# Optimization experiments

Hardware: AMD Instinct MI355X
Metric: run time of the kernel (lower is better)

Reference implementation:

```python
import jax, jax.numpy as jnp
import numpy as np

N = 10000      # nodes
E = 320000     # edges
H = 128        # hidden_features
GF = 12        # graph-level features
L = 6          # gnn layers
EPS = 1e-5


def _glorot(key, shape):
    fan_in = shape[0]
    return (jax.random.normal(key, shape, jnp.float32) / np.sqrt(fan_in)).astype(jnp.float32)


def periodic_difference(x_i, x_j, domain):
    diff = x_i - x_j
    # (1 - 2*(x_i < x_j)) * domain  ==  +domain if x_i >= x_j else -domain
    shift = jnp.where(x_i < x_j, -domain, domain)
    diff_shifted = diff - shift
    return jnp.where(jnp.abs(diff) < jnp.abs(diff_shifted), diff, diff_shifted)


def _mlp2_relu(x, W1, b1, W2, b2):
    # Linear -> ReLU -> Linear -> ReLU
    return jax.nn.relu(jax.nn.relu(x @ W1 + b1) @ W2 + b2)


def setup_inputs() -> dict:
    key = jax.random.key(0)
    ks = jax.random.split(key, 32)
    inp = {
        "v": jax.random.normal(ks[0], (N, 6), jnp.float32),
        "pos": jax.random.uniform(ks[1], (N, 3), jnp.float32),
        "r": jax.random.uniform(ks[2], (N, 1), jnp.float32),
        "domain": jnp.ones((3,), jnp.float32),
        "t": jax.random.uniform(ks[3], (1,), jnp.float32),
        "x_global": jax.random.normal(ks[4], (4,), jnp.float32),
        "domain_next": jnp.ones((3,), jnp.float32),
        "t_next": jax.random.uniform(ks[5], (1,), jnp.float32),
        "edge_index": jax.random.randint(ks[6], (2, E), 0, N, jnp.int32),
        "batch": jnp.zeros((N,), jnp.int32),
    }
    # embedding MLP: 19 -> H -> H
    inp["emb_W1"] = _glorot(ks[7], (19, H)); inp["emb_b1"] = jnp.zeros((H,), jnp.float32)
    inp["emb_W2"] = _glorot(ks[8], (H, H)); inp["emb_b2"] = jnp.zeros((H,), jnp.float32)
    # per-layer message net: 157 -> H -> H ; update net: 268 -> H -> H
    msg_in = H + GF + 3 + 2 * (6 + 1)   # 157
    upd_in = H + H + GF                 # 268
    inp["msg_W1"] = jnp.stack([_glorot(jax.random.fold_in(ks[9], i), (msg_in, H)) for i in range(L)])
    inp["msg_b1"] = jnp.zeros((L, H), jnp.float32)
    inp["msg_W2"] = jnp.stack([_glorot(jax.random.fold_in(ks[10], i), (H, H)) for i in range(L)])
    inp["msg_b2"] = jnp.zeros((L, H), jnp.float32)
    inp["upd_W1"] = jnp.stack([_glorot(jax.random.fold_in(ks[11], i), (upd_in, H)) for i in range(L)])
    inp["upd_b1"] = jnp.zeros((L, H), jnp.float32)
    inp["upd_W2"] = jnp.stack([_glorot(jax.random.fold_in(ks[12], i), (H, H)) for i in range(L)])
    inp["upd_b2"] = jnp.zeros((L, H), jnp.float32)
    # output MLP: H -> H -> 9 ; macro MLP: H -> H -> 3
    inp["out_W1"] = _glorot(ks[13], (H, H)); inp["out_b1"] = jnp.zeros((H,), jnp.float32)
    inp["out_W2"] = _glorot(ks[14], (H, 9)); inp["out_b2"] = jnp.zeros((9,), jnp.float32)
    inp["mac_W1"] = _glorot(ks[15], (H, H)); inp["mac_b1"] = jnp.zeros((H,), jnp.float32)
    inp["mac_W2"] = _glorot(ks[16], (H, 3)); inp["mac_b2"] = jnp.zeros((3,), jnp.float32)
    return inp


def reference(v, pos, r, domain, t, x_global, domain_next, t_next, edge_index, batch,
              emb_W1, emb_b1, emb_W2, emb_b2,
              msg_W1, msg_b1, msg_W2, msg_b2,
              upd_W1, upd_b1, upd_W2, upd_b2,
              out_W1, out_b1, out_W2, out_b2,
              mac_W1, mac_b1, mac_W2, mac_b2):
    n = v.shape[0]
    gf = jnp.concatenate([domain, t, x_global, domain_next, t_next])          # [12]
    gf_n = jnp.broadcast_to(gf, (n, GF))
    node_features = jnp.concatenate([pos, v], axis=1)                         # [N, 9]

    # embedding (positions excluded)
    h = _mlp2_relu(jnp.concatenate([r, v, gf_n], axis=1), emb_W1, emb_b1, emb_W2, emb_b2)

    src, dst = edge_index[0], edge_index[1]   # j = source, i = target (PyG default)
    gf_e = jnp.broadcast_to(gf, (src.shape[0], GF))
    counts = jax.ops.segment_sum(jnp.ones(src.shape, h.dtype), dst, num_segments=N)
    inv_counts = (1.0 / jnp.maximum(counts, 1.0))[:, None]

    pos_diff = periodic_difference(pos[dst], pos[src], domain)                # [E, 3]
    v_i, v_j, r_i, r_j = v[dst], v[src], r[dst], r[src]

    for l in range(L):
        h_i, h_j = h[dst], h[src]
        msg_in = jnp.concatenate([h_i - h_j, v_i, v_j, r_i, r_j, pos_diff, gf_e], axis=1)
        m = _mlp2_relu(msg_in, msg_W1[l], msg_b1[l], msg_W2[l], msg_b2[l])    # [E, H]
        agg = jax.ops.segment_sum(m, dst, num_segments=N) * inv_counts        # scatter-mean
        upd_in = jnp.concatenate([h, agg, gf_n], axis=1)
        u = _mlp2_relu(upd_in, upd_W1[l], upd_b1[l], upd_W2[l], upd_b2[l])
        h = u + h                                                              # residual (in==out)
        # InstanceNorm over each graph (single graph here), biased variance
        mu = h.mean(axis=0, keepdims=True)
        var = h.var(axis=0, keepdims=True)
        h = (h - mu) / jnp.sqrt(var + EPS)

    prediction = jax.nn.relu(h @ out_W1 + out_b1) @ out_W2 + out_b2 + node_features
    pred_x = jnp.remainder(prediction[:, :3], domain_next)
    pred_v = prediction[:, 3:]
    h_mean = h.mean(axis=0)                                                    # global mean pool, 1 graph
    pred_macro = jax.nn.relu(h_mean @ mac_W1 + mac_b1) @ mac_W2 + mac_b2
    return pred_x, pred_v, pred_macro
```

## Files before the change

kernel.cpp:

```cpp
#include <hip/hip_runtime.h>
#include <hip/hip_bf16.h>

#define NN 10000
#define NE 320000
#define HD 128
#define NL 6
#define EPSV 1e-5f

typedef _Float16 half8  __attribute__((ext_vector_type(8)));
typedef _Float16 half4v __attribute__((ext_vector_type(4)));
typedef __fp16   pk2    __attribute__((ext_vector_type(2)));
typedef float    f32x4  __attribute__((ext_vector_type(4)));

__device__ __forceinline__ float relu_(float x){ return fmaxf(x, 0.0f); }

#define LGKM_BAR() do { asm volatile("s_waitcnt lgkmcnt(0)" ::: "memory"); __builtin_amdgcn_s_barrier(); } while(0)

__device__ __forceinline__ void stats_(const float* __restrict__ s, const float* __restrict__ q,
                                       int idx, float& m, float& rs){
  m = s[idx]*(1.0f/NN);
  float var = q[idx]*(1.0f/NN) - m*m;
  rs = rsqrtf(fmaxf(var,0.0f)+EPSV);
}

__device__ __forceinline__ void pksplit4_(const f32x4& a, uint2& hi, uint2& lo){
  pk2 ha = __builtin_amdgcn_cvt_pkrtz(a[0], a[1]);
  pk2 hb = __builtin_amdgcn_cvt_pkrtz(a[2], a[3]);
  pk2 la = __builtin_amdgcn_cvt_pkrtz(a[0]-(float)ha[0], a[1]-(float)ha[1]);
  pk2 lb = __builtin_amdgcn_cvt_pkrtz(a[2]-(float)hb[0], a[3]-(float)hb[1]);
  hi.x = __builtin_bit_cast(unsigned int, ha);
  hi.y = __builtin_bit_cast(unsigned int, hb);
  lo.x = __builtin_bit_cast(unsigned int, la);
  lo.y = __builtin_bit_cast(unsigned int, lb);
}


__global__ void k_degree(const int* __restrict__ dst, int* __restrict__ counts){
  int e = blockIdx.x*256 + threadIdx.x;
  if (e < NE) atomicAdd(&counts[dst[e]], 1);
}

__global__ void k_scan(const int* __restrict__ counts, int* __restrict__ offs, float* __restrict__ invc){
  __shared__ int lds[1024];
  __shared__ int base_s;
  int tid = threadIdx.x;
  if (tid==0) base_s = 0;
  __syncthreads();
  for (int start=0; start<NN; start+=1024){
    int i = start+tid;
    int vv = (i<NN)? counts[i] : 0;
    lds[tid]=vv; __syncthreads();
    for (int off=1; off<1024; off<<=1){
      int t = (tid>=off)? lds[tid-off] : 0;
      __syncthreads();
      lds[tid] += t;
      __syncthreads();
    }
    int incl = lds[tid];
    if (i<NN){
      offs[i] = base_s + incl - vv;
      invc[i] = 1.0f / fmaxf((float)vv, 1.0f);
    }
    __syncthreads();
    if (tid==1023) base_s += lds[1023];
    __syncthreads();
  }
  if (tid==0) offs[NN] = base_s;
}

__global__ void k_place(const int* __restrict__ src, const int* __restrict__ dst,
                        const int* __restrict__ offs, int* __restrict__ cursor, int* __restrict__ csr){
  int e = blockIdx.x*256 + threadIdx.x;
  if (e < NE){
    int d = dst[e];
    int p = atomicAdd(&cursor[d], 1);
    csr[offs[d]+p] = src[e];
  }
}


__global__ void k_biasfold(const float* __restrict__ dom, const float* __restrict__ tt,
                           const float* __restrict__ xg, const float* __restrict__ domn,
                           const float* __restrict__ tn,
                           const float* __restrict__ embW1, const float* __restrict__ embB1,
                           const float* __restrict__ msgW1, const float* __restrict__ msgB1,
                           const float* __restrict__ updW1, const float* __restrict__ updB1,
                           float* __restrict__ b1eff, float* __restrict__ s0, float* __restrict__ q0){
  float gf[12];
  gf[0]=dom[0]; gf[1]=dom[1]; gf[2]=dom[2]; gf[3]=tt[0];
  gf[4]=xg[0]; gf[5]=xg[1]; gf[6]=xg[2]; gf[7]=xg[3];
  gf[8]=domn[0]; gf[9]=domn[1]; gf[10]=domn[2]; gf[11]=tn[0];
  int b = blockIdx.x, t = threadIdx.x;
  if (b==0){
    float s = embB1[t];
    #pragma unroll
    for (int k=0;k<12;++k) s += gf[k]*embW1[(7+k)*HD + t];
    b1eff[t] = s;
  } else if (b<=6){
    int l=b-1;
    float s = msgB1[l*HD+t];
    #pragma unroll
    for (int k=0;k<12;++k) s += gf[k]*msgW1[((size_t)l*157 + 145+k)*HD + t];
    b1eff[(1+l)*HD + t] = s;
  } else if (b<=12){
    int l=b-7;
    float s = updB1[l*HD+t];
    #pragma unroll
    for (int k=0;k<12;++k) s += gf[k]*updW1[((size_t)l*268 + 256+k)*HD + t];
    b1eff[(7+l)*HD + t] = s;
  } else {
    s0[t] = 0.f;
    q0[t] = (float)NN * (1.0f - EPSV);
  }
}


__global__ __launch_bounds__(512,1) void k_embed(
    const float* __restrict__ r, const float* __restrict__ v,
    const float* __restrict__ W1, const float* __restrict__ b1e,
    const float* __restrict__ W2, const float* __restrict__ b2,
    float* __restrict__ hb){
  __shared__ alignas(16) _Float16 Ahi[16*136];
  __shared__ alignas(16) _Float16 Alo[16*136];
  int tid = threadIdx.x;
  int n0 = blockIdx.x*16;
  if (tid < 256){
    int node = tid>>4, chunk = tid&15;
    int n = n0 + node;
    int f = chunk*8;
    float in7[7];
    in7[0]=r[n];
    #pragma unroll
    for (int k=0;k<6;++k) in7[1+k]=v[n*6+k];
    half8 ah, al;
    #pragma unroll
    for (int j=0;j<8;++j){
      float z = b1e[f+j];
      #pragma unroll
      for (int k=0;k<7;++k) z += in7[k]*W1[k*HD + f+j];
      float a = fmaxf(z, 0.f);
      _Float16 h = (_Float16)a;
      ah[j] = h; al[j] = (_Float16)(a - (float)h);
    }
    *(half8*)&Ahi[node*136 + f] = ah;
    *(half8*)&Alo[node*136 + f] = al;
  }
  int wid = tid>>6, lane = tid&63, g = lane>>4, c = lane&15;
  int col = 16*wid + c;
  half8 bh[4], bl[4];
  #pragma unroll
  for (int ks=0; ks<4; ++ks){
    half8 fh, fl;
    #pragma unroll
    for (int j=0;j<8;++j){
      float w = W2[(size_t)(ks*32 + g*8 + j)*HD + col];
      _Float16 h = (_Float16)w;
      fh[j]=h; fl[j]=(_Float16)(w - (float)h);
    }
    bh[ks]=fh; bl[ks]=fl;
  }
  float b2c = b2[col];
  f32x4 zero4 = {0.f,0.f,0.f,0.f};
  __syncthreads();
  f32x4 d = zero4;
  #pragma unroll
  for (int ks=0; ks<4; ++ks){
    half8 ah = *(const half8*)&Ahi[c*136 + ks*32 + g*8];
    half8 al = *(const half8*)&Alo[c*136 + ks*32 + g*8];
    d = __builtin_amdgcn_mfma_f32_16x16x32_f16(ah, bh[ks], d, 0,0,0);
    d = __builtin_amdgcn_mfma_f32_16x16x32_f16(al, bh[ks], d, 0,0,0);
    d = __builtin_amdgcn_mfma_f32_16x16x32_f16(ah, bl[ks], d, 0,0,0);
  }
  #pragma unroll
  for (int jj=0;jj<4;++jj){
    int n = n0 + g*4 + jj;
    hb[(size_t)n*HD + col] = fmaxf(d[jj] + b2c, 0.f);
  }
}


__global__ __launch_bounds__(512,1) void k_hW(
    const float* __restrict__ hb, const float* __restrict__ Ss, const float* __restrict__ Sq,
    const float* __restrict__ v, const float* __restrict__ r,
    const float* __restrict__ W, const float* __restrict__ b1e,
    float* __restrict__ P, float* __restrict__ Q){
  __shared__ alignas(16) _Float16 Xhi[16*136];
  __shared__ alignas(16) _Float16 Xlo[16*136];
  int tid = threadIdx.x;
  int n0 = blockIdx.x*16;
  if (tid < 256){
    int node = tid>>4, chunk = tid&15;
    int n = n0 + node;
    int f = chunk*8;
    half8 xh, xl;
    #pragma unroll
    for (int j=0;j<8;++j){
      float m, rs; stats_(Ss, Sq, f+j, m, rs);
      float x = (hb[(size_t)n*HD + f+j] - m) * rs;
      _Float16 h = (_Float16)x;
      xh[j] = h; xl[j] = (_Float16)(x - (float)h);
    }
    *(half8*)&Xhi[node*136 + f] = xh;
    *(half8*)&Xlo[node*136 + f] = xl;
  }
  int wid = tid>>6, lane = tid&63, g = lane>>4, c = lane&15;
  int col = 16*wid + c;
  half8 bh[4], bl[4];
  #pragma unroll
  for (int ks=0; ks<4; ++ks){
    half8 fh, fl;
    #pragma unroll
    for (int j=0;j<8;++j){
      float w = W[(size_t)(ks*32 + g*8 + j)*HD + col];
      _Float16 h = (_Float16)w;
      fh[j]=h; fl[j]=(_Float16)(w - (float)h);
    }
    bh[ks]=fh; bl[ks]=fl;
  }
  float wvi[6], wvj[6];
  #pragma unroll
  for (int x=0;x<6;++x){
    wvi[x]=W[(size_t)(128+x)*HD+col];
    wvj[x]=W[(size_t)(134+x)*HD+col];
  }
  float wri=W[(size_t)140*HD+col], wrj=W[(size_t)141*HD+col];
  float b1c=b1e[col];
  f32x4 zero4 = {0.f,0.f,0.f,0.f};
  __syncthreads();
  f32x4 d = zero4;
  #pragma unroll
  for (int ks=0; ks<4; ++ks){
    half8 ah = *(const half8*)&Xhi[c*136 + ks*32 + g*8];
    half8 al = *(const half8*)&Xlo[c*136 + ks*32 + g*8];
    d = __builtin_amdgcn_mfma_f32_16x16x32_f16(ah, bh[ks], d, 0,0,0);
    d = __builtin_amdgcn_mfma_f32_16x16x32_f16(al, bh[ks], d, 0,0,0);
    d = __builtin_amdgcn_mfma_f32_16x16x32_f16(ah, bl[ks], d, 0,0,0);
  }
  #pragma unroll
  for (int jj=0;jj<4;++jj){
    int n = n0 + g*4 + jj;
    float m = d[jj];
    float p = m + b1c, q = -m;
    #pragma unroll
    for (int x=0;x<6;++x){
      float vx = v[n*6+x];
      p += vx*wvi[x]; q += vx*wvj[x];
    }
    float rn = r[n];
    p += rn*wri; q += rn*wrj;
    P[(size_t)n*HD+col]=p;
    Q[(size_t)n*HD+col]=q;
  }
}


__global__ __launch_bounds__(256,2) void k_edge(
    const float* __restrict__ P, const float* __restrict__ Q,
    const float* __restrict__ pos, const float* __restrict__ dom,
    const int* __restrict__ offs, const int* __restrict__ csr,
    const float* __restrict__ Wpd, const float* __restrict__ W2, const float* __restrict__ b2,
    const float* __restrict__ invc, float* __restrict__ agg,
    float* __restrict__ zsum, float* __restrict__ zsumsq){
  __shared__ alignas(16) _Float16 a1hi[16*136];
  __shared__ alignas(16) _Float16 a1lo[16*136];
  int tid = threadIdx.x;
  if (blockIdx.x==0 && tid<HD){ zsum[tid]=0.f; zsumsq[tid]=0.f; }
  int wid = tid>>6, lane = tid&63, g = lane>>4, c = lane&15;
  int t0 = 2*wid, t1 = 2*wid+1;
  half8 w1f0, w1f1;
  {
    int fA = 16*t0 + c, fB = 16*t1 + c;
    float a0=Wpd[0*HD+fA], a1v=Wpd[1*HD+fA], a2v=Wpd[2*HD+fA];
    float b0=Wpd[0*HD+fB], b1v=Wpd[1*HD+fB], b2vv=Wpd[2*HD+fB];
    #pragma unroll
    for (int j=0;j<8;++j){ w1f0[j]=(_Float16)0.f; w1f1[j]=(_Float16)0.f; }
    if (g==0){
      _Float16 h0=(_Float16)a0, h1=(_Float16)a1v, h2=(_Float16)a2v;
      w1f0[0]=h0; w1f0[1]=h1; w1f0[2]=h2;
      w1f0[3]=h0; w1f0[4]=h1; w1f0[5]=h2;
      w1f0[6]=(_Float16)(a0-(float)h0);
      w1f0[7]=(_Float16)(a1v-(float)h1);
      _Float16 k0=(_Float16)b0, k1=(_Float16)b1v, k2=(_Float16)b2vv;
      w1f1[0]=k0; w1f1[1]=k1; w1f1[2]=k2;
      w1f1[3]=k0; w1f1[4]=k1; w1f1[5]=k2;
      w1f1[6]=(_Float16)(b0-(float)k0);
      w1f1[7]=(_Float16)(b1v-(float)k1);
    } else if (g==1){
      _Float16 h2=(_Float16)a2v, k2=(_Float16)b2vv;
      w1f0[0]=(_Float16)(a2v-(float)h2);
      w1f1[0]=(_Float16)(b2vv-(float)k2);
    }
  }
  half8 w2h[4][2], w2l[4][2];
  #pragma unroll
  for (int ks=0; ks<4; ++ks){
    #pragma unroll
    for (int tt=0; tt<2; ++tt){
      int col = 16*(2*wid+tt) + c;
      half8 fh, fl;
      #pragma unroll
      for (int j=0;j<8;++j){
        float w = W2[(ks*32 + g*8 + j)*HD + col];
        _Float16 h = (_Float16)w;
        fh[j] = h;
        fl[j] = (_Float16)(w - (float)h);
      }
      w2h[ks][tt] = fh;
      w2l[ks][tt] = fl;
    }
  }
  float b2v0 = b2[16*t0 + c], b2v1 = b2[16*t1 + c];
  float dm0=dom[0], dm1=dom[1], dm2=dom[2];
  f32x4 zero4 = {0.f,0.f,0.f,0.f};
  int n0 = blockIdx.x*2;
  for (int n = n0; n < n0+2; ++n){
    f32x4 pv0 = *(const f32x4*)(P + (size_t)n*HD + 16*t0 + 4*g);
    f32x4 pv1 = *(const f32x4*)(P + (size_t)n*HD + 16*t1 + 4*g);
    float pn0=pos[n*3+0], pn1=pos[n*3+1], pn2=pos[n*3+2];
    float acc0=0.f, acc1=0.f;
    int ib=offs[n], ie=offs[n+1];
    int sA_c=0; float qc0=0.f,qc1=0.f,qc2=0.f; f32x4 qv0_c=zero4, qv1_c=zero4;
    if (ib < ie){
      int nb0 = ie-ib; if (nb0>16) nb0=16;
      sA_c = csr[ib + ((c<nb0)? c : nb0-1)];
      qc0=pos[sA_c*3+0]; qc1=pos[sA_c*3+1]; qc2=pos[sA_c*3+2];
      qv0_c = *(const f32x4*)(Q + (size_t)sA_c*HD + 16*t0 + 4*g);
      qv1_c = *(const f32x4*)(Q + (size_t)sA_c*HD + 16*t1 + 4*g);
    }
    for (int base=ib; base<ie; base+=16){
      int nb = ie - base; if (nb>16) nb = 16;
      int bn = base + 16;
      int sA_n = 0;
      if (bn < ie){
        int nbn = ie - bn; if (nbn>16) nbn=16;
        sA_n = csr[bn + ((c<nbn)? c : nbn-1)];
      }
      float pd0,pd1,pd2;
      { float diff,sh,ds;
        diff=pn0-qc0; sh=(pn0<qc0)?-dm0:dm0; ds=diff-sh; pd0=(fabsf(diff)<fabsf(ds))?diff:ds;
        diff=pn1-qc1; sh=(pn1<qc1)?-dm1:dm1; ds=diff-sh; pd1=(fabsf(diff)<fabsf(ds))?diff:ds;
        diff=pn2-qc2; sh=(pn2<qc2)?-dm2:dm2; ds=diff-sh; pd2=(fabsf(diff)<fabsf(ds))?diff:ds;
      }
      _Float16 p0h = (_Float16)pd0, p1h = (_Float16)pd1, p2h = (_Float16)pd2;
      _Float16 p0l = (_Float16)(pd0 - (float)p0h);
      _Float16 p1l = (_Float16)(pd1 - (float)p1h);
      _Float16 p2l = (_Float16)(pd2 - (float)p2h);
      half8 pdf;
      #pragma unroll
      for (int j=0;j<8;++j) pdf[j]=(_Float16)0.f;
      if (g==0){ pdf[0]=p0h; pdf[1]=p1h; pdf[2]=p2h; pdf[3]=p0l; pdf[4]=p1l; pdf[5]=p2l; pdf[6]=p0h; pdf[7]=p1h; }
      else if (g==1){ pdf[0]=p2h; }
      f32x4 d0 = __builtin_amdgcn_mfma_f32_16x16x32_f16(w1f0, pdf, zero4, 0,0,0);
      f32x4 d1 = __builtin_amdgcn_mfma_f32_16x16x32_f16(w1f1, pdf, zero4, 0,0,0);
      f32x4 a0v, a1vv;
      #pragma unroll
      for (int j=0;j<4;++j){
        a0v[j]  = fmaxf(d0[j] + pv0[j] + qv0_c[j], 0.f);
        a1vv[j] = fmaxf(d1[j] + pv1[j] + qv1_c[j], 0.f);
      }
      uint2 h0, l0, h1, l1;
      pksplit4_(a0v,  h0, l0);
      pksplit4_(a1vv, h1, l1);
      *(uint2*)&a1hi[c*136 + 16*t0 + 4*g] = h0;
      *(uint2*)&a1lo[c*136 + 16*t0 + 4*g] = l0;
      *(uint2*)&a1hi[c*136 + 16*t1 + 4*g] = h1;
      *(uint2*)&a1lo[c*136 + 16*t1 + 4*g] = l1;
      LGKM_BAR();
      float qn0=0.f,qn1=0.f,qn2=0.f; f32x4 qv0_n=zero4, qv1_n=zero4;
      if (bn < ie){
        qn0=pos[sA_n*3+0]; qn1=pos[sA_n*3+1]; qn2=pos[sA_n*3+2];
        qv0_n = *(const f32x4*)(Q + (size_t)sA_n*HD + 16*t0 + 4*g);
        qv1_n = *(const f32x4*)(Q + (size_t)sA_n*HD + 16*t1 + 4*g);
      }
      f32x4 m0 = zero4, m1 = zero4;
      #pragma unroll
      for (int ks=0; ks<4; ++ks){
        half8 ah = *(const half8*)&a1hi[c*136 + ks*32 + g*8];
        half8 al = *(const half8*)&a1lo[c*136 + ks*32 + g*8];
        m0 = __builtin_amdgcn_mfma_f32_16x16x32_f16(ah, w2h[ks][0], m0, 0,0,0);
        m0 = __builtin_amdgcn_mfma_f32_16x16x32_f16(al, w2h[ks][0], m0, 0,0,0);
        m0 = __builtin_amdgcn_mfma_f32_16x16x32_f16(ah, w2l[ks][0], m0, 0,0,0);
        m1 = __builtin_amdgcn_mfma_f32_16x16x32_f16(ah, w2h[ks][1], m1, 0,0,0);
        m1 = __builtin_amdgcn_mfma_f32_16x16x32_f16(al, w2h[ks][1], m1, 0,0,0);
        m1 = __builtin_amdgcn_mfma_f32_16x16x32_f16(ah, w2l[ks][1], m1, 0,0,0);
      }
      if (nb == 16){
        acc0 += fmaxf(m0[0]+b2v0,0.f)+fmaxf(m0[1]+b2v0,0.f)+fmaxf(m0[2]+b2v0,0.f)+fmaxf(m0[3]+b2v0,0.f);
        acc1 += fmaxf(m1[0]+b2v1,0.f)+fmaxf(m1[1]+b2v1,0.f)+fmaxf(m1[2]+b2v1,0.f)+fmaxf(m1[3]+b2v1,0.f);
      } else {
        #pragma unroll
        for (int j=0;j<4;++j){
          if (4*g+j < nb){
            acc0 += fmaxf(m0[j]+b2v0, 0.f);
            acc1 += fmaxf(m1[j]+b2v1, 0.f);
          }
        }
      }
      LGKM_BAR();
      sA_c = sA_n; qc0=qn0; qc1=qn1; qc2=qn2; qv0_c=qv0_n; qv1_c=qv1_n;
    }
    acc0 += __shfl_xor(acc0, 16); acc0 += __shfl_xor(acc0, 32);
    acc1 += __shfl_xor(acc1, 16); acc1 += __shfl_xor(acc1, 32);
    if (g==0){
      float ic = invc[n];
      agg[n*HD + 16*t0 + c] = acc0*ic;
      agg[n*HD + 16*t1 + c] = acc1*ic;
    }
  }
}


__global__ __launch_bounds__(512,1) void k_upd(
    float* __restrict__ hb, const float* __restrict__ Ss, const float* __restrict__ Sq,
    const float* __restrict__ agg,
    const float* __restrict__ U1, const float* __restrict__ b1e,
    const float* __restrict__ U2, const float* __restrict__ bs2,
    float* __restrict__ sum, float* __restrict__ sumsq){
  __shared__ alignas(16) _Float16 Xhi[16*264];
  __shared__ alignas(16) _Float16 Xlo[16*264];
  __shared__ alignas(16) _Float16 Ahi[16*136];
  __shared__ alignas(16) _Float16 Alo[16*136];
  int tid = threadIdx.x;
  int n0 = blockIdx.x*16;
  {
    int node = tid>>5, chunk = tid&31;
    int n = n0 + node;
    int f = chunk*8;
    half8 xh, xl;
    if (f < 128){
      #pragma unroll
      for (int j=0;j<8;++j){
        float m, rs; stats_(Ss, Sq, f+j, m, rs);
        float x = (hb[(size_t)n*HD + f+j] - m) * rs;
        _Float16 h = (_Float16)x;
        xh[j] = h; xl[j] = (_Float16)(x - (float)h);
      }
    } else {
      #pragma unroll
      for (int j=0;j<8;++j){
        float x = agg[(size_t)n*HD + (f-128)+j];
        _Float16 h = (_Float16)x;
        xh[j] = h; xl[j] = (_Float16)(x - (float)h);
      }
    }
    *(half8*)&Xhi[node*264 + f] = xh;
    *(half8*)&Xlo[node*264 + f] = xl;
  }
  int wid = tid>>6, lane = tid&63, g = lane>>4, c = lane&15;
  int col = 16*wid + c;
  half8 b1h[8], b1l[8], b2h[4], b2l[4];
  #pragma unroll
  for (int ks=0; ks<8; ++ks){
    half8 fh, fl;
    #pragma unroll
    for (int j=0;j<8;++j){
      float w = U1[(size_t)(ks*32 + g*8 + j)*HD + col];
      _Float16 h = (_Float16)w;
      fh[j]=h; fl[j]=(_Float16)(w - (float)h);
    }
    b1h[ks]=fh; b1l[ks]=fl;
  }
  #pragma unroll
  for (int ks=0; ks<4; ++ks){
    half8 fh, fl;
    #pragma unroll
    for (int j=0;j<8;++j){
      float w = U2[(size_t)(ks*32 + g*8 + j)*HD + col];
      _Float16 h = (_Float16)w;
      fh[j]=h; fl[j]=(_Float16)(w - (float)h);
    }
    b2h[ks]=fh; b2l[ks]=fl;
  }
  f32x4 zero4 = {0.f,0.f,0.f,0.f};
  __syncthreads();
  f32x4 d = zero4;
  #pragma unroll
  for (int ks=0; ks<8; ++ks){
    half8 ah = *(const half8*)&Xhi[c*264 + ks*32 + g*8];
    half8 al = *(const half8*)&Xlo[c*264 + ks*32 + g*8];
    d = __builtin_amdgcn_mfma_f32_16x16x32_f16(ah, b1h[ks], d, 0,0,0);
    d = __builtin_amdgcn_mfma_f32_16x16x32_f16(al, b1h[ks], d, 0,0,0);
    d = __builtin_amdgcn_mfma_f32_16x16x32_f16(ah, b1l[ks], d, 0,0,0);
  }
  {
    float bb = b1e[col];
    #pragma unroll
    for (int jj=0;jj<4;++jj){
      float a = fmaxf(d[jj] + bb, 0.f);
      _Float16 h = (_Float16)a;
      Ahi[(g*4+jj)*136 + col] = h;
      Alo[(g*4+jj)*136 + col] = (_Float16)(a - (float)h);
    }
  }
  __syncthreads();
  f32x4 u = zero4;
  #pragma unroll
  for (int ks=0; ks<4; ++ks){
    half8 ah = *(const half8*)&Ahi[c*136 + ks*32 + g*8];
    half8 al = *(const half8*)&Alo[c*136 + ks*32 + g*8];
    u = __builtin_amdgcn_mfma_f32_16x16x32_f16(ah, b2h[ks], u, 0,0,0);
    u = __builtin_amdgcn_mfma_f32_16x16x32_f16(al, b2h[ks], u, 0,0,0);
    u = __builtin_amdgcn_mfma_f32_16x16x32_f16(ah, b2l[ks], u, 0,0,0);
  }
  float bc = bs2[col];
  float mc, rc; stats_(Ss, Sq, col, mc, rc);
  float s=0.f, q=0.f;
  #pragma unroll
  for (int jj=0;jj<4;++jj){
    int n = n0 + g*4 + jj;
    float hn = (hb[(size_t)n*HD + col] - mc)*rc;
    float b0 = hn + fmaxf(u[jj] + bc, 0.f);
    hb[(size_t)n*HD + col] = b0;
    s += b0; q += b0*b0;
  }
  s += __shfl_xor(s,16); s += __shfl_xor(s,32);
  q += __shfl_xor(q,16); q += __shfl_xor(q,32);
  if (g==0){
    atomicAdd(&sum[col], s);
    atomicAdd(&sumsq[col], q);
  }
}


__global__ __launch_bounds__(512,1) void k_out(
    const float* __restrict__ hb, const float* __restrict__ Ss, const float* __restrict__ Sq,
    const float* __restrict__ pos, const float* __restrict__ v,
    const float* __restrict__ W1, const float* __restrict__ b1,
    const float* __restrict__ W2, const float* __restrict__ b2,
    const float* __restrict__ domn, float* __restrict__ out){
  __shared__ alignas(16) _Float16 Xhi[16*136];
  __shared__ alignas(16) _Float16 Xlo[16*136];
  __shared__ alignas(16) _Float16 Ahi[16*136];
  __shared__ alignas(16) _Float16 Alo[16*136];
  int tid = threadIdx.x;
  int n0 = blockIdx.x*16;
  if (tid < 256){
    int node = tid>>4, chunk = tid&15;
    int n = n0 + node;
    int f = chunk*8;
    half8 xh, xl;
    #pragma unroll
    for (int j=0;j<8;++j){
      float m, rs; stats_(Ss, Sq, f+j, m, rs);
      float x = (hb[(size_t)n*HD + f+j] - m) * rs;
      _Float16 h = (_Float16)x;
      xh[j] = h; xl[j] = (_Float16)(x - (float)h);
    }
    *(half8*)&Xhi[node*136 + f] = xh;
    *(half8*)&Xlo[node*136 + f] = xl;
  }
  int wid = tid>>6, lane = tid&63, g = lane>>4, c = lane&15;
  int col = 16*wid + c;
  half8 bh[4], bl[4];
  #pragma unroll
  for (int ks=0; ks<4; ++ks){
    half8 fh, fl;
    #pragma unroll
    for (int j=0;j<8;++j){
      float w = W1[(size_t)(ks*32 + g*8 + j)*HD + col];
      _Float16 h = (_Float16)w;
      fh[j]=h; fl[j]=(_Float16)(w - (float)h);
    }
    bh[ks]=fh; bl[ks]=fl;
  }
  half8 w9h[4], w9l[4];
  if (wid==0){
    #pragma unroll
    for (int ks=0; ks<4; ++ks){
      half8 fh, fl;
      #pragma unroll
      for (int j=0;j<8;++j){
        float w = (c<9)? W2[(size_t)(ks*32 + g*8 + j)*9 + c] : 0.f;
        _Float16 h = (_Float16)w;
        fh[j]=h; fl[j]=(_Float16)(w - (float)h);
      }
      w9h[ks]=fh; w9l[ks]=fl;
    }
  }
  float b1c = b1[col];
  f32x4 zero4 = {0.f,0.f,0.f,0.f};
  __syncthreads();
  f32x4 d = zero4;
  #pragma unroll
  for (int ks=0; ks<4; ++ks){
    half8 ah = *(const half8*)&Xhi[c*136 + ks*32 + g*8];
    half8 al = *(const half8*)&Xlo[c*136 + ks*32 + g*8];
    d = __builtin_amdgcn_mfma_f32_16x16x32_f16(ah, bh[ks], d, 0,0,0);
    d = __builtin_amdgcn_mfma_f32_16x16x32_f16(al, bh[ks], d, 0,0,0);
    d = __builtin_amdgcn_mfma_f32_16x16x32_f16(ah, bl[ks], d, 0,0,0);
  }
  #pragma unroll
  for (int jj=0;jj<4;++jj){
    float a = fmaxf(d[jj] + b1c, 0.f);
    _Float16 h = (_Float16)a;
    Ahi[(g*4+jj)*136 + col] = h;
    Alo[(g*4+jj)*136 + col] = (_Float16)(a - (float)h);
  }
  __syncthreads();
  if (wid==0){
    f32x4 u = zero4;
    #pragma unroll
    for (int ks=0; ks<4; ++ks){
      half8 ah = *(const half8*)&Ahi[c*136 + ks*32 + g*8];
      half8 al = *(const half8*)&Alo[c*136 + ks*32 + g*8];
      u = __builtin_amdgcn_mfma_f32_16x16x32_f16(ah, w9h[ks], u, 0,0,0);
      u = __builtin_amdgcn_mfma_f32_16x16x32_f16(al, w9h[ks], u, 0,0,0);
      u = __builtin_amdgcn_mfma_f32_16x16x32_f16(ah, w9l[ks], u, 0,0,0);
    }
    if (c < 9){
      float bc = b2[c];
      #pragma unroll
      for (int jj=0;jj<4;++jj){
        int n = n0 + g*4 + jj;
        float p = u[jj] + bc;
        if (c < 3){
          p += pos[n*3+c];
          float dd = domn[c];
          p = p - floorf(p/dd)*dd;
          out[n*3+c] = p;
        } else {
          p += v[n*6 + (c-3)];
          out[3*NN + n*6 + (c-3)] = p;
        }
      }
    }
  }
}

__global__ void k_macro(const float* __restrict__ Ss, const float* __restrict__ Sq,
                        const float* __restrict__ W1, const float* __restrict__ b1,
                        const float* __restrict__ W2, const float* __restrict__ b2,
                        float* __restrict__ out){
  __shared__ float hm[HD];
  __shared__ float as[HD];
  int t=threadIdx.x;
  float m, rs; stats_(Ss, Sq, t, m, rs);
  hm[t] = (Ss[t]*(1.0f/NN) - m)*rs;
  __syncthreads();
  float z=b1[t];
  for (int k=0;k<HD;++k) z += hm[k]*W1[k*HD+t];
  as[t]=relu_(z);
  __syncthreads();
  if (t<3){
    float p=b2[t];
    for (int k=0;k<HD;++k) p += as[k]*W2[k*3+t];
    out[9*NN+t]=p;
  }
}


extern "C" void kernel_launch(void* const* d_in, const int* in_sizes, int n_in,
                              void* d_out, int out_size, void* d_ws, size_t ws_size,
                              hipStream_t stream) {
  const float* v    = (const float*)d_in[0];
  const float* pos  = (const float*)d_in[1];
  const float* r    = (const float*)d_in[2];
  const float* dom  = (const float*)d_in[3];
  const float* tt   = (const float*)d_in[4];
  const float* xg   = (const float*)d_in[5];
  const float* domn = (const float*)d_in[6];
  const float* tn   = (const float*)d_in[7];
  const int*   eidx = (const int*)d_in[8];
  const float* embW1 = (const float*)d_in[10];
  const float* embB1 = (const float*)d_in[11];
  const float* embW2 = (const float*)d_in[12];
  const float* embB2 = (const float*)d_in[13];
  const float* msgW1 = (const float*)d_in[14];
  const float* msgB1 = (const float*)d_in[15];
  const float* msgW2 = (const float*)d_in[16];
  const float* msgB2 = (const float*)d_in[17];
  const float* updW1 = (const float*)d_in[18];
  const float* updB1 = (const float*)d_in[19];
  const float* updW2 = (const float*)d_in[20];
  const float* updB2 = (const float*)d_in[21];
  const float* outW1 = (const float*)d_in[22];
  const float* outB1 = (const float*)d_in[23];
  const float* outW2 = (const float*)d_in[24];
  const float* outB2 = (const float*)d_in[25];
  const float* macW1 = (const float*)d_in[26];
  const float* macB1 = (const float*)d_in[27];
  const float* macW2 = (const float*)d_in[28];
  const float* macB2 = (const float*)d_in[29];
  float* out = (float*)d_out;
  float* ws  = (float*)d_ws;

  float* hb    = ws;
  float* P     = ws + 1280000;
  float* Q     = ws + 2560000;
  float* agg   = ws + 3840000;
  float* invc  = ws + 5120000;
  float* b1eff = ws + 5130000;
  float* sumA   = ws + 5131664;
  float* sumsqA = ws + 5131792;
  float* sumB   = ws + 5131920;
  float* sumsqB = ws + 5132048;
  int* counts  = (int*)(ws + 5132304);
  int* offs    = counts + NN;
  int* cursor  = offs + NN + 1;
  int* csr     = cursor + NN;

  float* Ssum[2]   = { sumA, sumB };
  float* Ssumsq[2] = { sumsqA, sumsqB };

  const int* srcA = eidx;
  const int* dstA = eidx + NE;

  hipMemsetAsync(counts, 0, NN*sizeof(int), stream);
  hipMemsetAsync(cursor, 0, NN*sizeof(int), stream);

  k_degree<<<(NE+255)/256, 256, 0, stream>>>(dstA, counts);
  k_scan<<<1, 1024, 0, stream>>>(counts, offs, invc);
  k_place<<<(NE+255)/256, 256, 0, stream>>>(srcA, dstA, offs, cursor, csr);
  k_biasfold<<<14, 128, 0, stream>>>(dom, tt, xg, domn, tn, embW1, embB1, msgW1, msgB1, updW1, updB1,
                                     b1eff, Ssum[0], Ssumsq[0]);
  k_embed<<<625, 512, 0, stream>>>(r, v, embW1, b1eff, embW2, embB2, hb);

  for (int l=0; l<NL; ++l){
    int in = l & 1, outp = (l+1) & 1;
    k_hW<<<625,512,0,stream>>>(hb, Ssum[in], Ssumsq[in], v, r,
        msgW1 + (size_t)l*157*HD, b1eff + (1+l)*HD, P, Q);
    k_edge<<<5000,256,0,stream>>>(P, Q, pos, dom, offs, csr,
        msgW1 + ((size_t)l*157+142)*HD,
        msgW2 + (size_t)l*HD*HD, msgB2 + l*HD, invc, agg, Ssum[outp], Ssumsq[outp]);
    k_upd<<<625,512,0,stream>>>(hb, Ssum[in], Ssumsq[in], agg,
        updW1 + (size_t)l*268*HD, b1eff + (7+l)*HD,
        updW2 + (size_t)l*HD*HD, updB2 + l*HD, Ssum[outp], Ssumsq[outp]);
  }

  k_out<<<625,512,0,stream>>>(hb, Ssum[0], Ssumsq[0], pos, v, outW1, outB1, outW2, outB2, domn, out);
  k_macro<<<1,128,0,stream>>>(Ssum[0], Ssumsq[0], macW1, macB1, macW2, macB2, out);
}
```

Measured before the change: 845.7 us.

## Interleave two destination nodes per block in edge kernel with double LDS buffers

The edge kernel now processes its two destination nodes concurrently instead of one after the other. Each node gets its own LDS staging buffers, and each iteration runs one 16-edge chunk for each node. The barriers are placed so that one node's second-layer MFMA work can overlap with the other node's first-layer stores and gathers. The aim is to hide gather latency and barrier stalls, at the cost of more registers, double the LDS, and idle iterations when the two nodes have different degrees.

```diff
diff --git a/kernel.cpp b/kernel.cpp
--- a/kernel.cpp
+++ b/kernel.cpp
@@ -261,8 +261,10 @@
     const float* __restrict__ Wpd, const float* __restrict__ W2, const float* __restrict__ b2,
     const float* __restrict__ invc, float* __restrict__ agg,
     float* __restrict__ zsum, float* __restrict__ zsumsq){
-  __shared__ alignas(16) _Float16 a1hi[16*136];
-  __shared__ alignas(16) _Float16 a1lo[16*136];
+  __shared__ alignas(16) _Float16 a1hiA[16*136];
+  __shared__ alignas(16) _Float16 a1loA[16*136];
+  __shared__ alignas(16) _Float16 a1hiB[16*136];
+  __shared__ alignas(16) _Float16 a1loB[16*136];
   int tid = threadIdx.x;
   if (blockIdx.x==0 && tid<HD){ zsum[tid]=0.f; zsumsq[tid]=0.f; }
   int wid = tid>>6, lane = tid&63, g = lane>>4, c = lane&15;
@@ -312,39 +314,51 @@
   float b2v0 = b2[16*t0 + c], b2v1 = b2[16*t1 + c];
   float dm0=dom[0], dm1=dom[1], dm2=dom[2];
   f32x4 zero4 = {0.f,0.f,0.f,0.f};
-  int n0 = blockIdx.x*2;
-  for (int n = n0; n < n0+2; ++n){
-    f32x4 pv0 = *(const f32x4*)(P + (size_t)n*HD + 16*t0 + 4*g);
-    f32x4 pv1 = *(const f32x4*)(P + (size_t)n*HD + 16*t1 + 4*g);
-    float pn0=pos[n*3+0], pn1=pos[n*3+1], pn2=pos[n*3+2];
-    float acc0=0.f, acc1=0.f;
-    int ib=offs[n], ie=offs[n+1];
-    int sA_c=0; float qc0=0.f,qc1=0.f,qc2=0.f; f32x4 qv0_c=zero4, qv1_c=zero4;
-    if (ib < ie){
-      int nb0 = ie-ib; if (nb0>16) nb0=16;
-      sA_c = csr[ib + ((c<nb0)? c : nb0-1)];
-      qc0=pos[sA_c*3+0]; qc1=pos[sA_c*3+1]; qc2=pos[sA_c*3+2];
-      qv0_c = *(const f32x4*)(Q + (size_t)sA_c*HD + 16*t0 + 4*g);
-      qv1_c = *(const f32x4*)(Q + (size_t)sA_c*HD + 16*t1 + 4*g);
-    }
-    for (int base=ib; base<ie; base+=16){
-      int nb = ie - base; if (nb>16) nb = 16;
-      int bn = base + 16;
-      int sA_n = 0;
-      if (bn < ie){
-        int nbn = ie - bn; if (nbn>16) nbn=16;
-        sA_n = csr[bn + ((c<nbn)? c : nbn-1)];
-      }
+
+  int nA = blockIdx.x*2, nB = nA+1;
+  f32x4 pvA0 = *(const f32x4*)(P + (size_t)nA*HD + 16*t0 + 4*g);
+  f32x4 pvA1 = *(const f32x4*)(P + (size_t)nA*HD + 16*t1 + 4*g);
+  f32x4 pvB0 = *(const f32x4*)(P + (size_t)nB*HD + 16*t0 + 4*g);
+  f32x4 pvB1 = *(const f32x4*)(P + (size_t)nB*HD + 16*t1 + 4*g);
+  float pA0=pos[nA*3+0], pA1=pos[nA*3+1], pA2=pos[nA*3+2];
+  float pB0=pos[nB*3+0], pB1=pos[nB*3+1], pB2=pos[nB*3+2];
+  int ibA=offs[nA], ieA=offs[nA+1];
+  int ibB=offs[nB], ieB=offs[nB+1];
+  int baseA=ibA, baseB=ibB;
+  float accA0=0.f, accA1=0.f, accB0=0.f, accB1=0.f;
+  float qAx=0.f,qAy=0.f,qAz=0.f; f32x4 qvA0=zero4, qvA1=zero4;
+  float qBx=0.f,qBy=0.f,qBz=0.f; f32x4 qvB0=zero4, qvB1=zero4;
+  if (baseA < ieA){
+    int nb = ieA-baseA; if (nb>16) nb=16;
+    int s = csr[baseA + ((c<nb)? c : nb-1)];
+    qAx=pos[s*3+0]; qAy=pos[s*3+1]; qAz=pos[s*3+2];
+    qvA0 = *(const f32x4*)(Q + (size_t)s*HD + 16*t0 + 4*g);
+    qvA1 = *(const f32x4*)(Q + (size_t)s*HD + 16*t1 + 4*g);
+  }
+  if (baseB < ieB){
+    int nb = ieB-baseB; if (nb>16) nb=16;
+    int s = csr[baseB + ((c<nb)? c : nb-1)];
+    qBx=pos[s*3+0]; qBy=pos[s*3+1]; qBz=pos[s*3+2];
+    qvB0 = *(const f32x4*)(Q + (size_t)s*HD + 16*t0 + 4*g);
+    qvB1 = *(const f32x4*)(Q + (size_t)s*HD + 16*t1 + 4*g);
+  }
+  int itA = (ieA-ibA+15)>>4, itB = (ieB-ibB+15)>>4;
+  int iters = (itA>itB)? itA : itB;
+  for (int it=0; it<iters; ++it){
+    bool haveA = baseA < ieA;
+    bool haveB = baseB < ieB;
+    int nbA = 0, nbB = 0;
+    if (haveA){ nbA = ieA-baseA; if (nbA>16) nbA=16; }
+    if (haveB){ nbB = ieB-baseB; if (nbB>16) nbB=16; }
+    if (haveA){
       float pd0,pd1,pd2;
       { float diff,sh,ds;
-        diff=pn0-qc0; sh=(pn0<qc0)?-dm0:dm0; ds=diff-sh; pd0=(fabsf(diff)<fabsf(ds))?diff:ds;
-        diff=pn1-qc1; sh=(pn1<qc1)?-dm1:dm1; ds=diff-sh; pd1=(fabsf(diff)<fabsf(ds))?diff:ds;
-        diff=pn2-qc2; sh=(pn2<qc2)?-dm2:dm2; ds=diff-sh; pd2=(fabsf(diff)<fabsf(ds))?diff:ds;
-      }
-      _Float16 p0h = (_Float16)pd0, p1h = (_Float16)pd1, p2h = (_Float16)pd2;
-      _Float16 p0l = (_Float16)(pd0 - (float)p0h);
-      _Float16 p1l = (_Float16)(pd1 - (float)p1h);
-      _Float16 p2l = (_Float16)(pd2 - (float)p2h);
+        diff=pA0-qAx; sh=(pA0<qAx)?-dm0:dm0; ds=diff-sh; pd0=(fabsf(diff)<fabsf(ds))?diff:ds;
+        diff=pA1-qAy; sh=(pA1<qAy)?-dm1:dm1; ds=diff-sh; pd1=(fabsf(diff)<fabsf(ds))?diff:ds;
+        diff=pA2-qAz; sh=(pA2<qAz)?-dm2:dm2; ds=diff-sh; pd2=(fabsf(diff)<fabsf(ds))?diff:ds;
+      }
+      _Float16 p0h=(_Float16)pd0, p1h=(_Float16)pd1, p2h=(_Float16)pd2;
+      _Float16 p0l=(_Float16)(pd0-(float)p0h), p1l=(_Float16)(pd1-(float)p1h), p2l=(_Float16)(pd2-(float)p2h);
       half8 pdf;
       #pragma unroll
       for (int j=0;j<8;++j) pdf[j]=(_Float16)0.f;
@@ -355,28 +369,34 @@
       f32x4 a0v, a1vv;
       #pragma unroll
       for (int j=0;j<4;++j){
-        a0v[j]  = fmaxf(d0[j] + pv0[j] + qv0_c[j], 0.f);
-        a1vv[j] = fmaxf(d1[j] + pv1[j] + qv1_c[j], 0.f);
-      }
-      uint2 h0, l0, h1, l1;
-      pksplit4_(a0v,  h0, l0);
+        a0v[j]  = fmaxf(d0[j] + pvA0[j] + qvA0[j], 0.f);
+        a1vv[j] = fmaxf(d1[j] + pvA1[j] + qvA1[j], 0.f);
+      }
+      uint2 h0,l0,h1,l1;
+      pksplit4_(a0v, h0, l0);
       pksplit4_(a1vv, h1, l1);
-      *(uint2*)&a1hi[c*136 + 16*t0 + 4*g] = h0;
-      *(uint2*)&a1lo[c*136 + 16*t0 + 4*g] = l0;
-      *(uint2*)&a1hi[c*136 + 16*t1 + 4*g] = h1;
-      *(uint2*)&a1lo[c*136 + 16*t1 + 4*g] = l1;
-      LGKM_BAR();
-      float qn0=0.f,qn1=0.f,qn2=0.f; f32x4 qv0_n=zero4, qv1_n=zero4;
-      if (bn < ie){
-        qn0=pos[sA_n*3+0]; qn1=pos[sA_n*3+1]; qn2=pos[sA_n*3+2];
-        qv0_n = *(const f32x4*)(Q + (size_t)sA_n*HD + 16*t0 + 4*g);
-        qv1_n = *(const f32x4*)(Q + (size_t)sA_n*HD + 16*t1 + 4*g);
-      }
+      *(uint2*)&a1hiA[c*136 + 16*t0 + 4*g] = h0;
+      *(uint2*)&a1loA[c*136 + 16*t0 + 4*g] = l0;
+      *(uint2*)&a1hiA[c*136 + 16*t1 + 4*g] = h1;
+      *(uint2*)&a1loA[c*136 + 16*t1 + 4*g] = l1;
+    }
+    LGKM_BAR();
+    {
+      int bn = baseA + 16;
+      if (bn < ieA){
+        int nbn = ieA - bn; if (nbn>16) nbn=16;
+        int s = csr[bn + ((c<nbn)? c : nbn-1)];
+        qAx=pos[s*3+0]; qAy=pos[s*3+1]; qAz=pos[s*3+2];
+        qvA0 = *(const f32x4*)(Q + (size_t)s*HD + 16*t0 + 4*g);
+        qvA1 = *(const f32x4*)(Q + (size_t)s*HD + 16*t1 + 4*g);
+      }
+    }
+    if (haveA){
       f32x4 m0 = zero4, m1 = zero4;
       #pragma unroll
       for (int ks=0; ks<4; ++ks){
-        half8 ah = *(const half8*)&a1hi[c*136 + ks*32 + g*8];
-        half8 al = *(const half8*)&a1lo[c*136 + ks*32 + g*8];
+        half8 ah = *(const half8*)&a1hiA[c*136 + ks*32 + g*8];
+        half8 al = *(const half8*)&a1loA[c*136 + ks*32 + g*8];
         m0 = __builtin_amdgcn_mfma_f32_16x16x32_f16(ah, w2h[ks][0], m0, 0,0,0);
         m0 = __builtin_amdgcn_mfma_f32_16x16x32_f16(al, w2h[ks][0], m0, 0,0,0);
         m0 = __builtin_amdgcn_mfma_f32_16x16x32_f16(ah, w2l[ks][0], m0, 0,0,0);
@@ -384,28 +404,99 @@
         m1 = __builtin_amdgcn_mfma_f32_16x16x32_f16(al, w2h[ks][1], m1, 0,0,0);
         m1 = __builtin_amdgcn_mfma_f32_16x16x32_f16(ah, w2l[ks][1], m1, 0,0,0);
       }
-      if (nb == 16){
-        acc0 += fmaxf(m0[0]+b2v0,0.f)+fmaxf(m0[1]+b2v0,0.f)+fmaxf(m0[2]+b2v0,0.f)+fmaxf(m0[3]+b2v0,0.f);
-        acc1 += fmaxf(m1[0]+b2v1,0.f)+fmaxf(m1[1]+b2v1,0.f)+fmaxf(m1[2]+b2v1,0.f)+fmaxf(m1[3]+b2v1,0.f);
+      if (nbA == 16){
+        accA0 += fmaxf(m0[0]+b2v0,0.f)+fmaxf(m0[1]+b2v0,0.f)+fmaxf(m0[2]+b2v0,0.f)+fmaxf(m0[3]+b2v0,0.f);
+        accA1 += fmaxf(m1[0]+b2v1,0.f)+fmaxf(m1[1]+b2v1,0.f)+fmaxf(m1[2]+b2v1,0.f)+fmaxf(m1[3]+b2v1,0.f);
       } else {
         #pragma unroll
         for (int j=0;j<4;++j){
-          if (4*g+j < nb){
-            acc0 += fmaxf(m0[j]+b2v0, 0.f);
-            acc1 += fmaxf(m1[j]+b2v1, 0.f);
+          if (4*g+j < nbA){
+            accA0 += fmaxf(m0[j]+b2v0, 0.f);
+            accA1 += fmaxf(m1[j]+b2v1, 0.f);
           }
         }
       }
-      LGKM_BAR();
-      sA_c = sA_n; qc0=qn0; qc1=qn1; qc2=qn2; qv0_c=qv0_n; qv1_c=qv1_n;
-    }
-    acc0 += __shfl_xor(acc0, 16); acc0 += __shfl_xor(acc0, 32);
-    acc1 += __shfl_xor(acc1, 16); acc1 += __shfl_xor(acc1, 32);
-    if (g==0){
-      float ic = invc[n];
-      agg[n*HD + 16*t0 + c] = acc0*ic;
-      agg[n*HD + 16*t1 + c] = acc1*ic;
-    }
+    }
+    if (haveB){
+      float pd0,pd1,pd2;
+      { float diff,sh,ds;
+        diff=pB0-qBx; sh=(pB0<qBx)?-dm0:dm0; ds=diff-sh; pd0=(fabsf(diff)<fabsf(ds))?diff:ds;
+        diff=pB1-qBy; sh=(pB1<qBy)?-dm1:dm1; ds=diff-sh; pd1=(fabsf(diff)<fabsf(ds))?diff:ds;
+        diff=pB2-qBz; sh=(pB2<qBz)?-dm2:dm2; ds=diff-sh; pd2=(fabsf(diff)<fabsf(ds))?diff:ds;
+      }
+      _Float16 p0h=(_Float16)pd0, p1h=(_Float16)pd1, p2h=(_Float16)pd2;
+      _Float16 p0l=(_Float16)(pd0-(float)p0h), p1l=(_Float16)(pd1-(float)p1h), p2l=(_Float16)(pd2-(float)p2h);
+      half8 pdf;
+      #pragma unroll
+      for (int j=0;j<8;++j) pdf[j]=(_Float16)0.f;
+      if (g==0){ pdf[0]=p0h; pdf[1]=p1h; pdf[2]=p2h; pdf[3]=p0l; pdf[4]=p1l; pdf[5]=p2l; pdf[6]=p0h; pdf[7]=p1h; }
+      else if (g==1){ pdf[0]=p2h; }
+      f32x4 d0 = __builtin_amdgcn_mfma_f32_16x16x32_f16(w1f0, pdf, zero4, 0,0,0);
+      f32x4 d1 = __builtin_amdgcn_mfma_f32_16x16x32_f16(w1f1, pdf, zero4, 0,0,0);
+      f32x4 a0v, a1vv;
+      #pragma unroll
+      for (int j=0;j<4;++j){
+        a0v[j]  = fmaxf(d0[j] + pvB0[j] + qvB0[j], 0.f);
+        a1vv[j] = fmaxf(d1[j] + pvB1[j] + qvB1[j], 0.f);
+      }
+      uint2 h0,l0,h1,l1;
+      pksplit4_(a0v, h0, l0);
+      pksplit4_(a1vv, h1, l1);
+      *(uint2*)&a1hiB[c*136 + 16*t0 + 4*g] = h0;
+      *(uint2*)&a1loB[c*136 + 16*t0 + 4*g] = l0;
+      *(uint2*)&a1hiB[c*136 + 16*t1 + 4*g] = h1;
+      *(uint2*)&a1loB[c*136 + 16*t1 + 4*g] = l1;
+    }
+    LGKM_BAR();
+    {
+      int bn = baseB + 16;
+      if (bn < ieB){
+        int nbn = ieB - bn; if (nbn>16) nbn=16;
+        int s = csr[bn + ((c<nbn)? c : nbn-1)];
+        qBx=pos[s*3+0]; qBy=pos[s*3+1]; qBz=pos[s*3+2];
+        qvB0 = *(const f32x4*)(Q + (size_t)s*HD + 16*t0 + 4*g);
+        qvB1 = *(const f32x4*)(Q + (size_t)s*HD + 16*t1 + 4*g);
+      }
+    }
+    if (haveB){
+      f32x4 m0 = zero4, m1 = zero4;
+      #pragma unroll
+      for (int ks=0; ks<4; ++ks){
+        half8 ah = *(const half8*)&a1hiB[c*136 + ks*32 + g*8];
+        half8 al = *(const half8*)&a1loB[c*136 + ks*32 + g*8];
+        m0 = __builtin_amdgcn_mfma_f32_16x16x32_f16(ah, w2h[ks][0], m0, 0,0,0);
+        m0 = __builtin_amdgcn_mfma_f32_16x16x32_f16(al, w2h[ks][0], m0, 0,0,0);
+        m0 = __builtin_amdgcn_mfma_f32_16x16x32_f16(ah, w2l[ks][0], m0, 0,0,0);
+        m1 = __builtin_amdgcn_mfma_f32_16x16x32_f16(ah, w2h[ks][1], m1, 0,0,0);
+        m1 = __builtin_amdgcn_mfma_f32_16x16x32_f16(al, w2h[ks][1], m1, 0,0,0);
+        m1 = __builtin_amdgcn_mfma_f32_16x16x32_f16(ah, w2l[ks][1], m1, 0,0,0);
+      }
+      if (nbB == 16){
+        accB0 += fmaxf(m0[0]+b2v0,0.f)+fmaxf(m0[1]+b2v0,0.f)+fmaxf(m0[2]+b2v0,0.f)+fmaxf(m0[3]+b2v0,0.f);
+        accB1 += fmaxf(m1[0]+b2v1,0.f)+fmaxf(m1[1]+b2v1,0.f)+fmaxf(m1[2]+b2v1,0.f)+fmaxf(m1[3]+b2v1,0.f);
+      } else {
+        #pragma unroll
+        for (int j=0;j<4;++j){
+          if (4*g+j < nbB){
+            accB0 += fmaxf(m0[j]+b2v0, 0.f);
+            accB1 += fmaxf(m1[j]+b2v1, 0.f);
+          }
+        }
+      }
+    }
+    baseA += 16; baseB += 16;
+  }
+  accA0 += __shfl_xor(accA0, 16); accA0 += __shfl_xor(accA0, 32);
+  accA1 += __shfl_xor(accA1, 16); accA1 += __shfl_xor(accA1, 32);
+  accB0 += __shfl_xor(accB0, 16); accB0 += __shfl_xor(accB0, 32);
+  accB1 += __shfl_xor(accB1, 16); accB1 += __shfl_xor(accB1, 32);
+  if (g==0){
+    float icA = invc[nA];
+    agg[nA*HD + 16*t0 + c] = accA0*icA;
+    agg[nA*HD + 16*t1 + c] = accA1*icA;
+    float icB = invc[nB];
+    agg[nB*HD + 16*t0 + c] = accB0*icB;
+    agg[nB*HD + 16*t1 + c] = accB1*icB;
   }
 }
 
```

New measurement: 988.3 us. +16.9%, slower.
